# Kernel optimization log

Measured on AMD Instinct MI355X. Metric: run time of the kernel, lower is better.

## Reference

```python
import jax, jax.numpy as jnp
import numpy as np

N_HEADS = 16
LOCAL_WINDOW = 256
GLOBAL_WINDOW = 1024


def _block_mha(x, in_proj_w, in_proj_b, out_proj_w, out_proj_b, window, n_heads):
    """Non-overlapping sliding-window MHA, matching torch nn.MultiheadAttention math.

    x: [B, S, D]; windows are independent -> fold them into the batch dim and do
    one batched attention (block-diagonal attention over the sequence).
    """
    B, S, D = x.shape
    nw = S // window
    hd = D // n_heads
    xw = x.reshape(B * nw, window, D)
    # combined QKV projection: in_proj_w is [3D, D], torch applies x @ W^T + b
    qkv = xw @ in_proj_w.T + in_proj_b  # [B*nw, W, 3D]
    q, k, v = jnp.split(qkv, 3, axis=-1)
    q = q.reshape(B * nw, window, n_heads, hd)
    k = k.reshape(B * nw, window, n_heads, hd)
    v = v.reshape(B * nw, window, n_heads, hd)
    scale = 1.0 / np.sqrt(hd).astype(np.float32)
    scores = jnp.einsum('bqhd,bkhd->bhqk', q, k) * scale
    attn = jax.nn.softmax(scores, axis=-1)
    out = jnp.einsum('bhqk,bkhd->bqhd', attn, v).reshape(B * nw, window, D)
    out = out @ out_proj_w.T + out_proj_b
    return out.reshape(B, S, D)


def setup_inputs() -> dict:
    key = jax.random.key(0)
    ks = jax.random.split(key, 8)
    B, S, D = 2, 4096, 1024
    w_scale = 1.0 / np.sqrt(D).astype(np.float32)
    return {
        'lqs': jax.random.normal(ks[0], (B, S, D), dtype=jnp.float32),
        'gqs': jax.random.normal(ks[1], (B, S, D), dtype=jnp.float32),
        'in_proj_w_l': jax.random.normal(ks[2], (3 * D, D), dtype=jnp.float32) * w_scale,
        'in_proj_b_l': jnp.zeros((3 * D,), dtype=jnp.float32),
        'out_proj_w_l': jax.random.normal(ks[3], (D, D), dtype=jnp.float32) * w_scale,
        'out_proj_b_l': jnp.zeros((D,), dtype=jnp.float32),
        'in_proj_w_g': jax.random.normal(ks[4], (3 * D, D), dtype=jnp.float32) * w_scale,
        'in_proj_b_g': jnp.zeros((3 * D,), dtype=jnp.float32),
        'out_proj_w_g': jax.random.normal(ks[5], (D, D), dtype=jnp.float32) * w_scale,
        'out_proj_b_g': jnp.zeros((D,), dtype=jnp.float32),
    }


def reference(lqs, gqs, in_proj_w_l, in_proj_b_l, out_proj_w_l, out_proj_b_l,
              in_proj_w_g, in_proj_b_g, out_proj_w_g, out_proj_b_g):
    local_out = _block_mha(lqs, in_proj_w_l, in_proj_b_l, out_proj_w_l, out_proj_b_l,
                           LOCAL_WINDOW, N_HEADS)
    global_out = _block_mha(gqs, in_proj_w_g, in_proj_b_g, out_proj_w_g, out_proj_b_g,
                            GLOBAL_WINDOW, N_HEADS)
    return (local_out, global_out)
```

## Files before the change

### kernel.cpp

```cpp
#include <hip/hip_runtime.h>
#include <stdint.h>

typedef __attribute__((ext_vector_type(8))) __bf16 bf16x8;
typedef __attribute__((ext_vector_type(4))) float f32x4;

__device__ __forceinline__ void async_ld16(const void* g, void* l) {
  __builtin_amdgcn_global_load_lds(
      (const __attribute__((address_space(1))) unsigned int*)g,
      (__attribute__((address_space(3))) unsigned int*)l, 16, 0, 0);
}

__device__ __forceinline__ unsigned short f2bf(float x) {
  union { float f; unsigned int u; } v; v.f = x;
  unsigned int r = v.u + 0x7FFFu + ((v.u >> 16) & 1u);
  return (unsigned short)(r >> 16);
}

__device__ __forceinline__ float exp2_fast(float x) {
  return __builtin_amdgcn_exp2f(x);
}

__device__ __forceinline__ unsigned int pack_bf2(float a, float b) {
  unsigned int ua = __builtin_bit_cast(unsigned int, a) + 0x8000u;
  unsigned int ub = __builtin_bit_cast(unsigned int, b) + 0x8000u;
  return __builtin_amdgcn_perm(ub, ua, 0x07060302u);
}

__global__ void cvt3(const float* __restrict__ x, unsigned short* __restrict__ xd,
                     const float* __restrict__ w1, unsigned short* __restrict__ w1d,
                     const float* __restrict__ w2, unsigned short* __restrict__ w2d) {
  int i = blockIdx.x * 256 + threadIdx.x;
  const float* s; unsigned short* d; int off;
  if (i < 2097152)      { s = x;  d = xd;  off = i; }
  else if (i < 2883584) { s = w1; d = w1d; off = i - 2097152; }
  else                  { s = w2; d = w2d; off = i - 2883584; }
  float4 v = ((const float4*)s)[off];
  ushort4 o;
  o.x = f2bf(v.x); o.y = f2bf(v.y); o.z = f2bf(v.z); o.w = f2bf(v.w);
  ((ushort4*)d)[off] = o;
}

__global__ __launch_bounds__(512, 2)
void gemm_bt(const unsigned short* __restrict__ A0, const unsigned short* __restrict__ A1,
             const unsigned short* __restrict__ B0, const unsigned short* __restrict__ B1,
             const float* __restrict__ bias0, const float* __restrict__ bias1,
             void* __restrict__ out0, void* __restrict__ out1,
             int N, int K, int f32out, int qlim, float qs) {
  __shared__ unsigned short As[2][2][256 * 32];
  __shared__ unsigned short Bs[2][2][256 * 32];
  int br = blockIdx.z;
  const unsigned short* A = br ? A1 : A0;
  const unsigned short* B = br ? B1 : B0;
  const float* bias = br ? bias1 : bias0;
  void* outp = br ? out1 : out0;

  int gx = gridDim.x, gy = gridDim.y;
  int nwg = gx * gy;
  int flat = blockIdx.y * gx + blockIdx.x;
  int cpx = nwg >> 3;
  int swb = (flat & 7) * cpx + (flat >> 3);
  int bxi = swb % gx, byi = swb / gx;

  int tid = threadIdx.x;
  int wave = tid >> 6, lane = tid & 63;
  int quad = lane >> 4, l16 = lane & 15;
  int wm = (wave >> 2) * 128;
  int wn = (wave & 3) * 64;
  size_t bm = (size_t)byi * 256, bn = (size_t)bxi * 256;

  f32x4 acc[8][4];
  f32x4 zero = {0.f, 0.f, 0.f, 0.f};
#pragma unroll
  for (int i = 0; i < 8; i++)
#pragma unroll
    for (int j = 0; j < 4; j++) acc[i][j] = zero;

  int swc = (quad ^ ((l16 >> 1) & 3)) * 16;
  const char* ArdB = (const char*)As + (wm + l16) * 64 + swc;
  const char* BrdB = (const char*)Bs + (wn + l16) * 64 + swc;

  int row0 = tid >> 2, c0 = (tid & 3) ^ ((row0 >> 1) & 3);
  int row1 = row0 + 128, c1 = (tid & 3) ^ ((row1 >> 1) & 3);
  const char* Ag0 = (const char*)(A + (bm + row0) * (size_t)K) + c0 * 16;
  const char* Ag1 = (const char*)(A + (bm + row1) * (size_t)K) + c1 * 16;
  const char* Bg0 = (const char*)(B + (bn + row0) * (size_t)K) + c0 * 16;
  const char* Bg1 = (const char*)(B + (bn + row1) * (size_t)K) + c1 * 16;
  char* ldsA = (char*)As + tid * 16;
  char* ldsB = (char*)Bs + tid * 16;

#define STAGE_A(po_, kh_, koff_) do {                    \
    char* d_ = ldsA + (po_) + (kh_) * 16384;             \
    async_ld16(Ag0 + (koff_), d_);                       \
    async_ld16(Ag1 + (koff_), d_ + 8192); } while (0)
#define STAGE_B(po_, kh_, koff_) do {                    \
    char* d_ = ldsB + (po_) + (kh_) * 16384;             \
    async_ld16(Bg0 + (koff_), d_);                       \
    async_ld16(Bg1 + (koff_), d_ + 8192); } while (0)
#define LDA_F(po_, kh_, mi_) (*(const bf16x8*)(ArdB + (po_) + (kh_) * 16384 + (mi_) * 1024))
#define LDB_F(po_, kh_, ni_) (*(const bf16x8*)(BrdB + (po_) + (kh_) * 16384 + (ni_) * 1024))
#define BAR() do { __builtin_amdgcn_s_barrier(); asm volatile("" ::: "memory"); } while (0)
#define MFMAQ(mb_, B0_, B1_, B2_, B3_, A0_, A1_, A2_, A3_) do {                                        \
    acc[(mb_)+0][0] = __builtin_amdgcn_mfma_f32_16x16x32_bf16(B0_, A0_, acc[(mb_)+0][0], 0, 0, 0);     \
    acc[(mb_)+1][0] = __builtin_amdgcn_mfma_f32_16x16x32_bf16(B0_, A1_, acc[(mb_)+1][0], 0, 0, 0);     \
    acc[(mb_)+2][0] = __builtin_amdgcn_mfma_f32_16x16x32_bf16(B0_, A2_, acc[(mb_)+2][0], 0, 0, 0);     \
    acc[(mb_)+3][0] = __builtin_amdgcn_mfma_f32_16x16x32_bf16(B0_, A3_, acc[(mb_)+3][0], 0, 0, 0);     \
    acc[(mb_)+0][1] = __builtin_amdgcn_mfma_f32_16x16x32_bf16(B1_, A0_, acc[(mb_)+0][1], 0, 0, 0);     \
    acc[(mb_)+1][1] = __builtin_amdgcn_mfma_f32_16x16x32_bf16(B1_, A1_, acc[(mb_)+1][1], 0, 0, 0);     \
    acc[(mb_)+2][1] = __builtin_amdgcn_mfma_f32_16x16x32_bf16(B1_, A2_, acc[(mb_)+2][1], 0, 0, 0);     \
    acc[(mb_)+3][1] = __builtin_amdgcn_mfma_f32_16x16x32_bf16(B1_, A3_, acc[(mb_)+3][1], 0, 0, 0);     \
    acc[(mb_)+0][2] = __builtin_amdgcn_mfma_f32_16x16x32_bf16(B2_, A0_, acc[(mb_)+0][2], 0, 0, 0);     \
    acc[(mb_)+1][2] = __builtin_amdgcn_mfma_f32_16x16x32_bf16(B2_, A1_, acc[(mb_)+1][2], 0, 0, 0);     \
    acc[(mb_)+2][2] = __builtin_amdgcn_mfma_f32_16x16x32_bf16(B2_, A2_, acc[(mb_)+2][2], 0, 0, 0);     \
    acc[(mb_)+3][2] = __builtin_amdgcn_mfma_f32_16x16x32_bf16(B2_, A3_, acc[(mb_)+3][2], 0, 0, 0);     \
    acc[(mb_)+0][3] = __builtin_amdgcn_mfma_f32_16x16x32_bf16(B3_, A0_, acc[(mb_)+0][3], 0, 0, 0);     \
    acc[(mb_)+1][3] = __builtin_amdgcn_mfma_f32_16x16x32_bf16(B3_, A1_, acc[(mb_)+1][3], 0, 0, 0);     \
    acc[(mb_)+2][3] = __builtin_amdgcn_mfma_f32_16x16x32_bf16(B3_, A2_, acc[(mb_)+2][3], 0, 0, 0);     \
    acc[(mb_)+3][3] = __builtin_amdgcn_mfma_f32_16x16x32_bf16(B3_, A3_, acc[(mb_)+3][3], 0, 0, 0);     \
  } while (0)

  const int NT = K >> 6;

  bf16x8 bX0, bX1, bX2, bX3;
  bf16x8 bY0, bY1, bY2, bY3;
  bf16x8 aP0, aP1, aP2, aP3;
  bf16x8 aQ0, aQ1, aQ2, aQ3;

  STAGE_A(0, 0, 0);       STAGE_B(0, 0, 0);
  STAGE_A(0, 1, 64);      STAGE_B(0, 1, 64);
  STAGE_A(32768, 0, 128); STAGE_B(32768, 0, 128);
  STAGE_A(32768, 1, 192);
  asm volatile("s_waitcnt vmcnt(10)" ::: "memory");
  BAR();
  bX0 = LDB_F(0, 0, 0); bX1 = LDB_F(0, 0, 1); bX2 = LDB_F(0, 0, 2); bX3 = LDB_F(0, 0, 3);
  aP0 = LDA_F(0, 0, 0); aP1 = LDA_F(0, 0, 1); aP2 = LDA_F(0, 0, 2); aP3 = LDA_F(0, 0, 3);

  for (int j = 0; j < NT; ++j) {
    int po = (j & 1) * 32768;
    int qo = po ^ 32768;
    int ko1 = ((j + 1 < NT) ? j + 1 : NT - 1) * 128;
    int ko2 = ((j + 2 < NT) ? j + 2 : NT - 1) * 128;

    aQ0 = LDA_F(po, 0, 4); aQ1 = LDA_F(po, 0, 5); aQ2 = LDA_F(po, 0, 6); aQ3 = LDA_F(po, 0, 7);
    STAGE_B(qo, 1, ko1 + 64);
    __builtin_amdgcn_s_setprio(1);
    MFMAQ(0, bX0, bX1, bX2, bX3, aP0, aP1, aP2, aP3);
    __builtin_amdgcn_s_setprio(0);
    asm volatile("s_waitcnt vmcnt(8)" ::: "memory");
    BAR();
    bY0 = LDB_F(po, 1, 0); bY1 = LDB_F(po, 1, 1); bY2 = LDB_F(po, 1, 2); bY3 = LDB_F(po, 1, 3);
    aP0 = LDA_F(po, 1, 0); aP1 = LDA_F(po, 1, 1); aP2 = LDA_F(po, 1, 2); aP3 = LDA_F(po, 1, 3);
    STAGE_A(po, 0, ko2);
    __builtin_amdgcn_s_setprio(1);
    MFMAQ(4, bX0, bX1, bX2, bX3, aQ0, aQ1, aQ2, aQ3);
    __builtin_amdgcn_s_setprio(0);
    BAR();
    aQ0 = LDA_F(po, 1, 4); aQ1 = LDA_F(po, 1, 5); aQ2 = LDA_F(po, 1, 6); aQ3 = LDA_F(po, 1, 7);
    STAGE_B(po, 0, ko2);
    __builtin_amdgcn_s_setprio(1);
    MFMAQ(0, bY0, bY1, bY2, bY3, aP0, aP1, aP2, aP3);
    __builtin_amdgcn_s_setprio(0);
    asm volatile("s_waitcnt vmcnt(8)" ::: "memory");
    BAR();
    bX0 = LDB_F(qo, 0, 0); bX1 = LDB_F(qo, 0, 1); bX2 = LDB_F(qo, 0, 2); bX3 = LDB_F(qo, 0, 3);
    aP0 = LDA_F(qo, 0, 0); aP1 = LDA_F(qo, 0, 1); aP2 = LDA_F(qo, 0, 2); aP3 = LDA_F(qo, 0, 3);
    STAGE_A(po, 1, ko2 + 64);
    __builtin_amdgcn_s_setprio(1);
    MFMAQ(4, bY0, bY1, bY2, bY3, aQ0, aQ1, aQ2, aQ3);
    __builtin_amdgcn_s_setprio(0);
    BAR();
  }

#undef STAGE_A
#undef STAGE_B
#undef LDA_F
#undef LDB_F
#undef BAR
#undef MFMAQ

#pragma unroll
  for (int mi = 0; mi < 8; mi++) {
    size_t rowg = bm + wm + mi * 16 + l16;
#pragma unroll
    for (int ni = 0; ni < 4; ni++) {
      size_t col = bn + wn + ni * 16 + quad * 4;
      float s = ((int)col < qlim) ? qs : 1.0f;
      float4 bv = *(const float4*)&bias[col];
      f32x4 a = acc[mi][ni];
      if (f32out) {
        float4 o = {(a[0] + bv.x) * s, (a[1] + bv.y) * s,
                    (a[2] + bv.z) * s, (a[3] + bv.w) * s};
        *(float4*)&((float*)outp)[rowg * N + col] = o;
      } else {
        ushort4 o;
        o.x = f2bf((a[0] + bv.x) * s); o.y = f2bf((a[1] + bv.y) * s);
        o.z = f2bf((a[2] + bv.z) * s); o.w = f2bf((a[3] + bv.w) * s);
        *(ushort4*)&((unsigned short*)outp)[rowg * N + col] = o;
      }
    }
  }
}

__device__ __forceinline__ int kperm(int p) {
  return (p & 0xC3) | ((p & 0x0C) << 2) | ((p & 0x30) >> 2);
}
__global__ void transpose_v(const unsigned short* __restrict__ q0, unsigned short* __restrict__ v0, int W0,
                            const unsigned short* __restrict__ q1, unsigned short* __restrict__ v1, int W1,
                            int zsplit) {
  __shared__ unsigned short tile[64][33];
  int z = blockIdx.z;
  const unsigned short* qkv; unsigned short* vt; int W, wb, yy;
  if (z < zsplit) { qkv = q0; vt = v0; W = W0; wb = z; yy = blockIdx.y; }
  else { qkv = q1; vt = v1; W = W1; int t = z - zsplit; wb = t >> 2; yy = blockIdx.y + 4 * (t & 3); }
  int c0 = blockIdx.x * 32, w0 = yy * 64;
  const unsigned short* src = qkv + (size_t)wb * W * 3072 + 2048;
  for (int i = threadIdx.y; i < 64; i += 8)
    tile[i][threadIdx.x] = src[(size_t)(w0 + i) * 3072 + c0 + threadIdx.x];
  __syncthreads();
  unsigned short* dst = vt + (size_t)wb * 1024 * W;
  for (int i = threadIdx.y; i < 32; i += 8) {
    int p0 = threadIdx.x, p1 = threadIdx.x + 32;
    dst[(size_t)(c0 + i) * W + w0 + p0] = tile[kperm(p0)][i];
    dst[(size_t)(c0 + i) * W + w0 + p1] = tile[kperm(p1)][i];
  }
}

__global__ __launch_bounds__(256)
void attn_fused(const unsigned short* __restrict__ qkv0, const unsigned short* __restrict__ vt0,
                unsigned short* __restrict__ ao0, int W0, int nb0,
                const unsigned short* __restrict__ qkv1, const unsigned short* __restrict__ vt1,
                unsigned short* __restrict__ ao1, int W1) {
  __shared__ unsigned short Ks[64 * 64];
  __shared__ unsigned short Vs[64 * 64];
  __shared__ unsigned int   Ps[4][16 * 32];
  int bid = blockIdx.x;
  const unsigned short *qkv, *vtb0; unsigned short* ao; int W, rel;
  if (bid < nb0) { qkv = qkv0; vtb0 = vt0; ao = ao0; W = W0; rel = bid; }
  else           { qkv = qkv1; vtb0 = vt1; ao = ao1; W = W1; rel = bid - nb0; }
  int gx = W >> 7;
  int shift = (gx == 2) ? 1 : 3;
  int bx = rel & (gx - 1);
  int wbh = rel >> shift;
  int wb = wbh >> 4, h = wbh & 15;

  int tid = threadIdx.x;
  int wave = tid >> 6, lane = tid & 63;
  int quad = lane >> 4, l16 = lane & 15;
  int swz = l16 & 7;
  int q0w = bx * 128 + wave * 32;

  const unsigned short* qb = qkv + (size_t)wb * W * 3072 + h * 64;
  const unsigned short* kb = qb + 1024;
  const unsigned short* vtb = vtb0 + (size_t)wbh * 64 * W;

  bf16x8 qf[2][2];
  for (int cb = 0; cb < 2; cb++)
    for (int ch = 0; ch < 2; ch++)
      qf[cb][ch] = *(const bf16x8*)(qb + (size_t)(q0w + cb * 16 + l16) * 3072 +
                                    ch * 32 + quad * 8);

  f32x4 zero = {0.f, 0.f, 0.f, 0.f};
  f32x4 O[2][4];
  for (int cb = 0; cb < 2; cb++)
    for (int g = 0; g < 4; g++) O[cb][g] = zero;
  float l_i[2] = {0.f, 0.f};

  for (int k0 = 0; k0 < W; k0 += 64) {
    __syncthreads();
    for (int j = 0; j < 2; j++) {
      int c = j * 256 + tid;
      int row = c >> 3, sl = c & 7, ss = sl ^ (row & 7);
      async_ld16(kb + (size_t)(k0 + row) * 3072 + ss * 8, (char*)Ks + c * 16);
      async_ld16(vtb + (size_t)row * W + k0 + ss * 8,     (char*)Vs + c * 16);
    }
    __syncthreads();

    bf16x8 ak[4][2], vf[4][2];
#pragma unroll
    for (int i = 0; i < 4; i++)
#pragma unroll
      for (int ch = 0; ch < 2; ch++) {
        int sl = (ch * 4 + quad) ^ swz;
        ak[i][ch] = *(const bf16x8*)&Ks[(i * 16 + l16) * 64 + sl * 8];
        vf[i][ch] = *(const bf16x8*)&Vs[(i * 16 + l16) * 64 + sl * 8];
      }

    for (int cb = 0; cb < 2; cb++) {
      unsigned int pk[8];
      float sm = 0.f;
#pragma unroll
      for (int sub = 0; sub < 4; sub++) {
        f32x4 z = zero;
        z = __builtin_amdgcn_mfma_f32_16x16x32_bf16(ak[sub][0], qf[cb][0], z, 0, 0, 0);
        z = __builtin_amdgcn_mfma_f32_16x16x32_bf16(ak[sub][1], qf[cb][1], z, 0, 0, 0);
        float p0 = exp2_fast(z[0]), p1 = exp2_fast(z[1]);
        float p2 = exp2_fast(z[2]), p3 = exp2_fast(z[3]);
        sm += (p0 + p1) + (p2 + p3);
        pk[((sub & 1) * 2) + (sub >> 1) * 4]     = pack_bf2(p0, p1);
        pk[((sub & 1) * 2) + (sub >> 1) * 4 + 1] = pack_bf2(p2, p3);
      }
      sm += __shfl_xor(sm, 16);
      sm += __shfl_xor(sm, 32);
      l_i[cb] += sm;

      unsigned int* pw = &Ps[wave][0];
      uint4 u0 = {pk[0], pk[1], pk[2], pk[3]};
      uint4 u1 = {pk[4], pk[5], pk[6], pk[7]};
      *(uint4*)&pw[l16 * 32 + ((2 * quad) ^ swz) * 4]     = u0;
      *(uint4*)&pw[l16 * 32 + ((2 * quad + 1) ^ swz) * 4] = u1;

      bf16x8 pf[2];
#pragma unroll
      for (int ch = 0; ch < 2; ch++) {
        uint4 u = *(const uint4*)&pw[l16 * 32 + ((ch * 4 + quad) ^ swz) * 4];
        pf[ch] = __builtin_bit_cast(bf16x8, u);
      }
#pragma unroll
      for (int g = 0; g < 4; g++) {
        O[cb][g] = __builtin_amdgcn_mfma_f32_16x16x32_bf16(pf[0], vf[g][0], O[cb][g], 0, 0, 0);
        O[cb][g] = __builtin_amdgcn_mfma_f32_16x16x32_bf16(pf[1], vf[g][1], O[cb][g], 0, 0, 0);
      }
    }
  }

  for (int cb = 0; cb < 2; cb++) {
    float inv = 1.0f / l_i[cb];
    float ivr[4];
    for (int r = 0; r < 4; r++) ivr[r] = __shfl(inv, quad * 4 + r);
    for (int r = 0; r < 4; r++) {
      size_t rowg = (size_t)wb * W + q0w + cb * 16 + quad * 4 + r;
      for (int g = 0; g < 4; g++)
        ao[rowg * 1024 + h * 64 + g * 16 + l16] = f2bf(O[cb][g][r] * ivr[r]);
    }
  }
}

extern "C" void kernel_launch(void* const* d_in, const int* in_sizes, int n_in,
                              void* d_out, int out_size, void* d_ws, size_t ws_size,
                              hipStream_t stream) {
  const int D = 1024, TD = 3072, M = 8192;
  const float QS = 0.125f * 1.44269504089f;
  const size_t PER = 46137344;
  bool comb = ws_size >= (size_t)2 * PER * 2;

  unsigned short* Xb[2]; unsigned short* Wb[2]; unsigned short* Ob[2];
  unsigned short* qkv[2]; unsigned short* vt[2];
  for (int b = 0; b < 2; b++) {
    unsigned short* base = (unsigned short*)d_ws + (comb ? b * PER : 0);
    Xb[b]  = base;
    Wb[b]  = Xb[b] + 8388608;
    Ob[b]  = Wb[b] + 3145728;
    qkv[b] = Ob[b] + 1048576;
    vt[b]  = qkv[b] + 25165824;
  }
  float* outp = (float*)d_out;
  const float* x[2]   = {(const float*)d_in[0], (const float*)d_in[1]};
  const float* ipw[2] = {(const float*)d_in[2], (const float*)d_in[6]};
  const float* ipb[2] = {(const float*)d_in[3], (const float*)d_in[7]};
  const float* opw[2] = {(const float*)d_in[4], (const float*)d_in[8]};
  const float* opb[2] = {(const float*)d_in[5], (const float*)d_in[9]};
  const int Wd[2] = {256, 1024};

  if (comb) {
    for (int b = 0; b < 2; b++)
      cvt3<<<12288, 256, 0, stream>>>(x[b], Xb[b], ipw[b], Wb[b], opw[b], Ob[b]);
    gemm_bt<<<dim3(TD / 256, M / 256, 2), 512, 0, stream>>>(
        Xb[0], Xb[1], Wb[0], Wb[1], ipb[0], ipb[1], qkv[0], qkv[1],
        TD, D, 0, D, QS);
    transpose_v<<<dim3(32, 4, 64), dim3(32, 8), 0, stream>>>(
        qkv[0], vt[0], 256, qkv[1], vt[1], 1024, 32);
    attn_fused<<<2048, 256, 0, stream>>>(
        qkv[0], vt[0], Xb[0], 256, 1024, qkv[1], vt[1], Xb[1], 1024);
    gemm_bt<<<dim3(D / 256, M / 256, 2), 512, 0, stream>>>(
        Xb[0], Xb[1], Ob[0], Ob[1], opb[0], opb[1], outp, outp + 8388608,
        D, D, 1, 0, 1.0f);
  } else {
    for (int b = 0; b < 2; b++) {
      int W = Wd[b], nwb = M / W;
      cvt3<<<12288, 256, 0, stream>>>(x[b], Xb[b], ipw[b], Wb[b], opw[b], Ob[b]);
      gemm_bt<<<dim3(TD / 256, M / 256, 1), 512, 0, stream>>>(
          Xb[b], Xb[b], Wb[b], Wb[b], ipb[b], ipb[b], qkv[b], qkv[b],
          TD, D, 0, D, QS);
      if (b == 0)
        transpose_v<<<dim3(32, 4, 32), dim3(32, 8), 0, stream>>>(
            qkv[b], vt[b], W, qkv[b], vt[b], W, 32);
      else
        transpose_v<<<dim3(32, 4, 32), dim3(32, 8), 0, stream>>>(
            qkv[b], vt[b], W, qkv[b], vt[b], W, 0);
      int nb = (W >> 7) * nwb * 16;
      attn_fused<<<nb, 256, 0, stream>>>(
          qkv[b], vt[b], Xb[b], W, nb, qkv[b], vt[b], Xb[b], W);
      gemm_bt<<<dim3(D / 256, M / 256, 1), 512, 0, stream>>>(
          Xb[b], Xb[b], Ob[b], Ob[b], opb[b], opb[b],
          outp + (size_t)b * 8388608, outp + (size_t)b * 8388608,
          D, D, 1, 0, 1.0f);
    }
  }
}
```

Baseline: 413.5 us.

## Simplify GEMM to plain double-buffer pipeline and double-buffer attention K/V tiles

The GEMM main loop drops its interleaved two-tile-ahead staging, with its partial vmcnt waits, mid-iteration barriers and setprio hints. In its place is a simple scheme: issue all loads for the next K tile, run four MFMA quads on the current buffer, then wait for vmcnt(0) and sync once. The attention kernel gains a second K/V shared-memory buffer, so the next tile's async loads are issued before computing on the current one, removing the second barrier per step. The GEMM change trades finer load/compute overlap and fewer stalls for simpler code and fewer barriers. The attention change costs double the K/V LDS, which may reduce occupancy.

```diff
diff --git a/kernel.cpp b/kernel.cpp
--- a/kernel.cpp
+++ b/kernel.cpp
@@ -120,53 +120,34 @@
 
   const int NT = K >> 6;
 
-  bf16x8 bX0, bX1, bX2, bX3;
-  bf16x8 bY0, bY1, bY2, bY3;
-  bf16x8 aP0, aP1, aP2, aP3;
-  bf16x8 aQ0, aQ1, aQ2, aQ3;
-
-  STAGE_A(0, 0, 0);       STAGE_B(0, 0, 0);
-  STAGE_A(0, 1, 64);      STAGE_B(0, 1, 64);
-  STAGE_A(32768, 0, 128); STAGE_B(32768, 0, 128);
-  STAGE_A(32768, 1, 192);
-  asm volatile("s_waitcnt vmcnt(10)" ::: "memory");
+  STAGE_A(0, 0, 0);  STAGE_B(0, 0, 0);
+  STAGE_A(0, 1, 64); STAGE_B(0, 1, 64);
+  asm volatile("s_waitcnt vmcnt(0)" ::: "memory");
   BAR();
-  bX0 = LDB_F(0, 0, 0); bX1 = LDB_F(0, 0, 1); bX2 = LDB_F(0, 0, 2); bX3 = LDB_F(0, 0, 3);
-  aP0 = LDA_F(0, 0, 0); aP1 = LDA_F(0, 0, 1); aP2 = LDA_F(0, 0, 2); aP3 = LDA_F(0, 0, 3);
 
   for (int j = 0; j < NT; ++j) {
     int po = (j & 1) * 32768;
     int qo = po ^ 32768;
-    int ko1 = ((j + 1 < NT) ? j + 1 : NT - 1) * 128;
-    int ko2 = ((j + 2 < NT) ? j + 2 : NT - 1) * 128;
-
+    int kn = ((j + 1 < NT) ? j + 1 : NT - 1) * 128;
+
+    STAGE_A(qo, 0, kn);      STAGE_B(qo, 0, kn);
+    STAGE_A(qo, 1, kn + 64); STAGE_B(qo, 1, kn + 64);
+
+    bf16x8 bX0, bX1, bX2, bX3, bY0, bY1, bY2, bY3;
+    bf16x8 aP0, aP1, aP2, aP3, aQ0, aQ1, aQ2, aQ3;
+
+    bX0 = LDB_F(po, 0, 0); bX1 = LDB_F(po, 0, 1); bX2 = LDB_F(po, 0, 2); bX3 = LDB_F(po, 0, 3);
+    aP0 = LDA_F(po, 0, 0); aP1 = LDA_F(po, 0, 1); aP2 = LDA_F(po, 0, 2); aP3 = LDA_F(po, 0, 3);
     aQ0 = LDA_F(po, 0, 4); aQ1 = LDA_F(po, 0, 5); aQ2 = LDA_F(po, 0, 6); aQ3 = LDA_F(po, 0, 7);
-    STAGE_B(qo, 1, ko1 + 64);
-    __builtin_amdgcn_s_setprio(1);
     MFMAQ(0, bX0, bX1, bX2, bX3, aP0, aP1, aP2, aP3);
-    __builtin_amdgcn_s_setprio(0);
-    asm volatile("s_waitcnt vmcnt(8)" ::: "memory");
-    BAR();
     bY0 = LDB_F(po, 1, 0); bY1 = LDB_F(po, 1, 1); bY2 = LDB_F(po, 1, 2); bY3 = LDB_F(po, 1, 3);
     aP0 = LDA_F(po, 1, 0); aP1 = LDA_F(po, 1, 1); aP2 = LDA_F(po, 1, 2); aP3 = LDA_F(po, 1, 3);
-    STAGE_A(po, 0, ko2);
-    __builtin_amdgcn_s_setprio(1);
     MFMAQ(4, bX0, bX1, bX2, bX3, aQ0, aQ1, aQ2, aQ3);
-    __builtin_amdgcn_s_setprio(0);
-    BAR();
     aQ0 = LDA_F(po, 1, 4); aQ1 = LDA_F(po, 1, 5); aQ2 = LDA_F(po, 1, 6); aQ3 = LDA_F(po, 1, 7);
-    STAGE_B(po, 0, ko2);
-    __builtin_amdgcn_s_setprio(1);
     MFMAQ(0, bY0, bY1, bY2, bY3, aP0, aP1, aP2, aP3);
-    __builtin_amdgcn_s_setprio(0);
-    asm volatile("s_waitcnt vmcnt(8)" ::: "memory");
-    BAR();
-    bX0 = LDB_F(qo, 0, 0); bX1 = LDB_F(qo, 0, 1); bX2 = LDB_F(qo, 0, 2); bX3 = LDB_F(qo, 0, 3);
-    aP0 = LDA_F(qo, 0, 0); aP1 = LDA_F(qo, 0, 1); aP2 = LDA_F(qo, 0, 2); aP3 = LDA_F(qo, 0, 3);
-    STAGE_A(po, 1, ko2 + 64);
-    __builtin_amdgcn_s_setprio(1);
     MFMAQ(4, bY0, bY1, bY2, bY3, aQ0, aQ1, aQ2, aQ3);
-    __builtin_amdgcn_s_setprio(0);
+
+    asm volatile("s_waitcnt vmcnt(0)" ::: "memory");
     BAR();
   }
 
@@ -229,8 +210,8 @@
                 unsigned short* __restrict__ ao0, int W0, int nb0,
                 const unsigned short* __restrict__ qkv1, const unsigned short* __restrict__ vt1,
                 unsigned short* __restrict__ ao1, int W1) {
-  __shared__ unsigned short Ks[64 * 64];
-  __shared__ unsigned short Vs[64 * 64];
+  __shared__ unsigned short Ks[2][64 * 64];
+  __shared__ unsigned short Vs[2][64 * 64];
   __shared__ unsigned int   Ps[4][16 * 32];
   int bid = blockIdx.x;
   const unsigned short *qkv, *vtb0; unsigned short* ao; int W, rel;
@@ -264,15 +245,29 @@
     for (int g = 0; g < 4; g++) O[cb][g] = zero;
   float l_i[2] = {0.f, 0.f};
 
-  for (int k0 = 0; k0 < W; k0 += 64) {
+  {
+    int c0s = tid, c1s = 256 + tid;
+    int r0 = c0s >> 3, s0 = (c0s & 7) ^ (r0 & 7);
+    int r1 = c1s >> 3, s1 = (c1s & 7) ^ (r1 & 7);
+    async_ld16(kb + (size_t)r0 * 3072 + s0 * 8, (char*)&Ks[0][0] + c0s * 16);
+    async_ld16(vtb + (size_t)r0 * W + s0 * 8,   (char*)&Vs[0][0] + c0s * 16);
+    async_ld16(kb + (size_t)r1 * 3072 + s1 * 8, (char*)&Ks[0][0] + c1s * 16);
+    async_ld16(vtb + (size_t)r1 * W + s1 * 8,   (char*)&Vs[0][0] + c1s * 16);
+  }
+
+  int it = 0;
+  for (int k0 = 0; k0 < W; k0 += 64, ++it) {
+    int cur = it & 1;
     __syncthreads();
-    for (int j = 0; j < 2; j++) {
-      int c = j * 256 + tid;
-      int row = c >> 3, sl = c & 7, ss = sl ^ (row & 7);
-      async_ld16(kb + (size_t)(k0 + row) * 3072 + ss * 8, (char*)Ks + c * 16);
-      async_ld16(vtb + (size_t)row * W + k0 + ss * 8,     (char*)Vs + c * 16);
-    }
-    __syncthreads();
+    if (k0 + 64 < W) {
+      int nxt = cur ^ 1, kk = k0 + 64;
+      for (int j = 0; j < 2; j++) {
+        int c = j * 256 + tid;
+        int row = c >> 3, sl = c & 7, ss = sl ^ (row & 7);
+        async_ld16(kb + (size_t)(kk + row) * 3072 + ss * 8, (char*)&Ks[nxt][0] + c * 16);
+        async_ld16(vtb + (size_t)row * W + kk + ss * 8,     (char*)&Vs[nxt][0] + c * 16);
+      }
+    }
 
     bf16x8 ak[4][2], vf[4][2];
 #pragma unroll
@@ -280,8 +275,8 @@
 #pragma unroll
       for (int ch = 0; ch < 2; ch++) {
         int sl = (ch * 4 + quad) ^ swz;
-        ak[i][ch] = *(const bf16x8*)&Ks[(i * 16 + l16) * 64 + sl * 8];
-        vf[i][ch] = *(const bf16x8*)&Vs[(i * 16 + l16) * 64 + sl * 8];
+        ak[i][ch] = *(const bf16x8*)&Ks[cur][(i * 16 + l16) * 64 + sl * 8];
+        vf[i][ch] = *(const bf16x8*)&Vs[cur][(i * 16 + l16) * 64 + sl * 8];
       }
 
     for (int cb = 0; cb < 2; cb++) {
```

Result: slower. 426.5 us (+3.2%).
